# Performance work log

Measured on AMD Instinct MI355X. Metric: run time of the kernel, lower is better.

## Reference

```python
import jax, jax.numpy as jnp
import numpy as np

B, T, IN, H, L, OUT = 64, 512, 128, 256, 3, 50
G = 3 * H  # gate dim (r,z,n)


def setup_inputs() -> dict:
    key = jax.random.key(0)
    ks = jax.random.split(key, 18)
    s = 0.08  # keep gates out of saturation
    r = jax.random.normal
    return {
        "x": r(ks[0], (B, T, IN), jnp.float32),
        "Wih0": r(ks[1], (2, G, IN)) * s,
        "Whh0": r(ks[2], (2, G, H)) * s,
        "bih0": r(ks[3], (2, G)) * s,
        "bhh0": r(ks[4], (2, G)) * s,
        "Wih": r(ks[5], (L - 1, 2, G, 2 * H)) * s,
        "Whh": r(ks[6], (L - 1, 2, G, H)) * s,
        "bih": r(ks[7], (L - 1, 2, G)) * s,
        "bhh": r(ks[8], (L - 1, 2, G)) * s,
        "W1": r(ks[9], (128, 2 * H)) * s,
        "b1": r(ks[10], (128,)) * s,
        "W2": r(ks[11], (64, 128)) * s,
        "b2": r(ks[12], (64,)) * s,
        "W3": r(ks[13], (H, 64)) * s,
        "b3": r(ks[14], (H,)) * s,
        "W4": r(ks[15], (OUT, H)) * s,
        "b4": r(ks[16], (OUT,)) * s,
    }


def _gru_dir(x, Wih, Whh, bih, bhh, reverse):
    # x: [B,T,D]. Precompute input gates with one big GEMM, scan only hidden matmul.
    xg = jnp.einsum('btd,gd->tbg', x, Wih) + bih  # [T,B,3H]
    h0 = jnp.zeros((x.shape[0], H), x.dtype)

    def step(h, xg_t):
        hg = h @ Whh.T + bhh                     # [B,3H]
        xr, xz, xn = jnp.split(xg_t, 3, axis=-1)
        hr, hz, hn = jnp.split(hg, 3, axis=-1)
        r = jax.nn.sigmoid(xr + hr)
        z = jax.nn.sigmoid(xz + hz)
        n = jnp.tanh(xn + r * hn)
        h = (1.0 - z) * n + z * h
        return h, h

    _, ys = jax.lax.scan(step, h0, xg, reverse=reverse)  # ys[t] aligned to time t
    return jnp.transpose(ys, (1, 0, 2))  # [B,T,H]


def reference(x, Wih0, Whh0, bih0, bhh0, Wih, Whh, bih, bhh,
              W1, b1, W2, b2, W3, b3, W4, b4):
    h = x
    for l in range(L):
        if l == 0:
            wi, wh, bi, bh = Wih0, Whh0, bih0, bhh0
        else:
            wi, wh, bi, bh = Wih[l - 1], Whh[l - 1], bih[l - 1], bhh[l - 1]
        fwd = _gru_dir(h, wi[0], wh[0], bi[0], bh[0], False)
        bwd = _gru_dir(h, wi[1], wh[1], bi[1], bh[1], True)
        h = jnp.concatenate([fwd, bwd], axis=-1)  # [B,T,2H]
    last = h[:, -1, :]  # [B,2H]
    y = jax.nn.relu(last @ W1.T + b1)
    y = jax.nn.relu(y @ W2.T + b2)
    y = jax.nn.relu(y @ W3.T + b3)
    return y @ W4.T + b4  # [B,OUT]
```

## Files before the change

### kernel.cpp

```cpp
#include <hip/hip_runtime.h>
#include <stdint.h>

#define B_ 64
#define T_ 512
#define IN_ 128
#define H_ 256
#define G_ 768
#define M0_ (B_*T_)

typedef _Float16 f16;
typedef _Float16 f16x2 __attribute__((ext_vector_type(2)));
typedef _Float16 half8 __attribute__((ext_vector_type(8)));
typedef float f32x4 __attribute__((ext_vector_type(4)));

template<bool AF32>
__global__ __launch_bounds__(256) void k_proj(
    const float* __restrict__ Af, const f16* __restrict__ Ah,
    const float* __restrict__ W, const float* __restrict__ bias,
    f16* __restrict__ out, int K)
{
  int dir = blockIdx.z;
  const float* Wd = W + (size_t)dir*G_*K;
  const float* bd = bias + dir*G_;
  f16* outd = out + (size_t)dir*M0_*G_;
  int m0 = blockIdx.x*128, n0 = blockIdx.y*128;
  int tid = threadIdx.x, lane = tid & 63, wv = tid >> 6;
  int wm = wv >> 1, wn = wv & 1;
  int l15 = lane & 15, quad = lane >> 4;

  __shared__ f16 As[128][72];
  __shared__ f16 Ws[128][72];

  f32x4 acc[4][4];
  #pragma unroll
  for (int i = 0; i < 4; i++)
    #pragma unroll
    for (int j = 0; j < 4; j++) acc[i][j] = (f32x4){0.f,0.f,0.f,0.f};

  int lr = tid >> 3, lk = (tid & 7) * 8;
  for (int k0 = 0; k0 < K; k0 += 64){
    #pragma unroll
    for (int it = 0; it < 4; it++){
      int row = lr + it*32;
      if (AF32){
        const float* p = &Af[(size_t)(m0+row)*K + k0 + lk];
        float4 v0 = *(const float4*)p;
        float4 v1 = *(const float4*)(p + 4);
        *(half8*)&As[row][lk] = (half8){(f16)v0.x,(f16)v0.y,(f16)v0.z,(f16)v0.w,
                                        (f16)v1.x,(f16)v1.y,(f16)v1.z,(f16)v1.w};
      } else {
        *(uint4*)&As[row][lk] = *(const uint4*)&Ah[(size_t)(m0+row)*K + k0 + lk];
      }
      {
        const float* p = &Wd[(size_t)(n0+row)*K + k0 + lk];
        float4 v0 = *(const float4*)p;
        float4 v1 = *(const float4*)(p + 4);
        *(half8*)&Ws[row][lk] = (half8){(f16)v0.x,(f16)v0.y,(f16)v0.z,(f16)v0.w,
                                        (f16)v1.x,(f16)v1.y,(f16)v1.z,(f16)v1.w};
      }
    }
    __syncthreads();
    #pragma unroll
    for (int kk = 0; kk < 64; kk += 32){
      half8 af[4], bf[4];
      #pragma unroll
      for (int mi = 0; mi < 4; mi++) af[mi] = *(const half8*)&As[wm*64 + mi*16 + l15][kk + quad*8];
      #pragma unroll
      for (int ni = 0; ni < 4; ni++) bf[ni] = *(const half8*)&Ws[wn*64 + ni*16 + l15][kk + quad*8];
      #pragma unroll
      for (int mi = 0; mi < 4; mi++)
        #pragma unroll
        for (int ni = 0; ni < 4; ni++)
          acc[mi][ni] = __builtin_amdgcn_mfma_f32_16x16x32_f16(af[mi], bf[ni], acc[mi][ni], 0, 0, 0);
    }
    __syncthreads();
  }
  #pragma unroll
  for (int mi = 0; mi < 4; mi++){
    #pragma unroll
    for (int ni = 0; ni < 4; ni++){
      int m = m0 + wm*64 + mi*16 + quad*4;
      int n = n0 + wn*64 + ni*16 + l15;
      float bn = bd[n];
      #pragma unroll
      for (int r = 0; r < 4; r++)
        outd[(size_t)(m+r)*G_ + n] = (f16)(acc[mi][ni][r] + bn);
    }
  }
}

__global__ __launch_bounds__(256) __attribute__((amdgpu_waves_per_eu(1, 1)))
void k_rnn(
    const f16* __restrict__ xg, const float* __restrict__ whh,
    const float* __restrict__ bhh, f16* __restrict__ y)
{
  int b = blockIdx.x, dir = blockIdx.y;
  int tid = threadIdx.x, lane = tid & 63, wv = tid >> 6;
  int kg = lane >> 4;

  const f16* cxg = xg + ((size_t)dir*M0_ + (size_t)b*T_)*G_;
  const float* wbase = whh + (size_t)dir*G_*H_;
  const float* bh = bhh + dir*G_;
  f16* yb = y + (size_t)b*T_*512 + dir*256;

  __shared__ __align__(16) f16 h0buf[256];
  __shared__ __align__(16) f16 h1buf[256];

  half8 wf[96];
  #pragma unroll
  for (int t = 0; t < 12; t++){
    int g = t >> 2, c = t & 3;
    const float* wrow = wbase + (size_t)(g*256 + wv*64 + c*16 + (lane & 15))*H_;
    #pragma unroll
    for (int kf = 0; kf < 8; kf++){
      const float4* p = (const float4*)(wrow + kf*32 + kg*8);
      float4 v0 = p[0], v1 = p[1];
      wf[t*8+kf] = (half8){(f16)v0.x,(f16)v0.y,(f16)v0.z,(f16)v0.w,
                           (f16)v1.x,(f16)v1.y,(f16)v1.z,(f16)v1.w};
    }
  }

  float br = bh[tid], bz = bh[tid+256], bn = bh[tid+512];
  float hreg = 0.f;
  h0buf[tid] = (f16)0.f;
  __syncthreads();

  f16 axr_, axz_, axn_, bxr_, bxz_, bxn_;

  {
    int t0 = dir ? (T_-1) : 0;
    const f16* xp = cxg + (size_t)t0*G_ + tid;
    axr_ = xp[0]; axz_ = xp[256]; axn_ = xp[512];
  }

#define STEP_BODY(SRC, DST, XR, XZ, XN, TT)                                     \
  {                                                                             \
    const f16* hp = &SRC[kg*8];                                                 \
    f32x4 acc[12];                                                              \
    half8 acur = *(const half8*)hp;                                             \
    half8 anxt = *(const half8*)(hp + 32);                                      \
    _Pragma("unroll")                                                           \
    for (int kf = 0; kf < 8; kf++){                                             \
      half8 ac = acur;                                                          \
      acur = anxt;                                                              \
      if (kf < 6) anxt = *(const half8*)(hp + (kf+2)*32);                       \
      _Pragma("unroll")                                                         \
      for (int t = 0; t < 12; t++){                                             \
        if (kf == 0)                                                            \
          acc[t] = __builtin_amdgcn_mfma_f32_16x16x32_f16(ac, wf[t*8+kf],       \
                     (f32x4){0.f,0.f,0.f,0.f}, 0, 0, 0);                        \
        else                                                                    \
          acc[t] = __builtin_amdgcn_mfma_f32_16x16x32_f16(ac, wf[t*8+kf],       \
                     acc[t], 0, 0, 0);                                          \
      }                                                                         \
    }                                                                           \
    float r0 = (kg & 1) ? acc[1][0] : acc[0][0];                                \
    float r1 = (kg & 1) ? acc[3][0] : acc[2][0];                                \
    float sr = (kg & 2) ? r1 : r0;                                              \
    float z0 = (kg & 1) ? acc[5][0] : acc[4][0];                                \
    float z1 = (kg & 1) ? acc[7][0] : acc[6][0];                                \
    float sz = (kg & 2) ? z1 : z0;                                              \
    float n0v = (kg & 1) ? acc[9][0]  : acc[8][0];                              \
    float n1v = (kg & 1) ? acc[11][0] : acc[10][0];                             \
    float sn = (kg & 2) ? n1v : n0v;                                            \
    float ar = (float)(XR) + sr + br; ar = fminf(fmaxf(ar, -30.f), 30.f);       \
    float az = (float)(XZ) + sz + bz; az = fminf(fmaxf(az, -30.f), 30.f);       \
    float r = 1.f/(1.f + __expf(-ar));                                          \
    float z = 1.f/(1.f + __expf(-az));                                          \
    float an = (float)(XN) + r*(sn + bn); an = fminf(fmaxf(an, -15.f), 15.f);   \
    float e = __expf(2.f*an);                                                   \
    float nn = (e - 1.f)/(e + 1.f);                                             \
    hreg = (1.f - z)*nn + z*hreg;                                               \
    DST[tid] = (f16)hreg;                                                       \
    yb[(size_t)(TT)*512 + tid] = (f16)hreg;                                     \
    asm volatile("s_waitcnt lgkmcnt(0)\n\ts_barrier" ::: "memory");             \
  }

  for (int s = 0; s < T_; s += 2){
    int ttA = dir ? (T_-1-s) : s;
    int ttB = dir ? (T_-2-s) : (s+1);

    {
      const f16* xq = cxg + (size_t)ttB*G_ + tid;
      bxr_ = xq[0]; bxz_ = xq[256]; bxn_ = xq[512];
    }
    STEP_BODY(h0buf, h1buf, axr_, axz_, axn_, ttA)

    {
      int s2 = (s + 2 < T_) ? (s + 2) : (T_ - 1);
      int tt2 = dir ? (T_-1-s2) : s2;
      const f16* xq = cxg + (size_t)tt2*G_ + tid;
      axr_ = xq[0]; axz_ = xq[256]; axn_ = xq[512];
    }
    STEP_BODY(h1buf, h0buf, bxr_, bxz_, bxn_, ttB)
  }
#undef STEP_BODY
}

__global__ __launch_bounds__(256) void k_head(
    const f16* __restrict__ y,
    const float* __restrict__ W1, const float* __restrict__ b1,
    const float* __restrict__ W2, const float* __restrict__ b2,
    const float* __restrict__ W3, const float* __restrict__ b3,
    const float* __restrict__ W4, const float* __restrict__ b4,
    float* __restrict__ out)
{
  int b = blockIdx.x, tid = threadIdx.x;
  __shared__ float a0[512], a1[128], a2[64], a3[256];
  const f16* yr = y + ((size_t)b*T_ + (T_-1))*512;
  a0[tid] = (float)yr[tid]; a0[tid+256] = (float)yr[tid+256];
  __syncthreads();
  if (tid < 128){
    float s = b1[tid];
    const float4* w = (const float4*)(W1 + (size_t)tid*512);
    #pragma unroll 8
    for (int c = 0; c < 128; c++){
      float4 v = w[c];
      s += v.x*a0[c*4] + v.y*a0[c*4+1] + v.z*a0[c*4+2] + v.w*a0[c*4+3];
    }
    a1[tid] = fmaxf(s, 0.f);
  }
  __syncthreads();
  if (tid < 64){
    float s = b2[tid];
    const float4* w = (const float4*)(W2 + (size_t)tid*128);
    #pragma unroll
    for (int c = 0; c < 32; c++){
      float4 v = w[c];
      s += v.x*a1[c*4] + v.y*a1[c*4+1] + v.z*a1[c*4+2] + v.w*a1[c*4+3];
    }
    a2[tid] = fmaxf(s, 0.f);
  }
  __syncthreads();
  if (tid < 256){
    float s = b3[tid];
    const float4* w = (const float4*)(W3 + (size_t)tid*64);
    #pragma unroll
    for (int c = 0; c < 16; c++){
      float4 v = w[c];
      s += v.x*a2[c*4] + v.y*a2[c*4+1] + v.z*a2[c*4+2] + v.w*a2[c*4+3];
    }
    a3[tid] = fmaxf(s, 0.f);
  }
  __syncthreads();
  if (tid < 50){
    float s = b4[tid];
    const float4* w = (const float4*)(W4 + (size_t)tid*256);
    #pragma unroll
    for (int c = 0; c < 64; c++){
      float4 v = w[c];
      s += v.x*a3[c*4] + v.y*a3[c*4+1] + v.z*a3[c*4+2] + v.w*a3[c*4+3];
    }
    out[b*50 + tid] = s;
  }
}

extern "C" void kernel_launch(void* const* d_in, const int* in_sizes, int n_in,
                              void* d_out, int out_size, void* d_ws, size_t ws_size,
                              hipStream_t stream)
{
  const float* x    = (const float*)d_in[0];
  const float* Wih0 = (const float*)d_in[1];
  const float* Whh0 = (const float*)d_in[2];
  const float* bih0 = (const float*)d_in[3];
  const float* bhh0 = (const float*)d_in[4];
  const float* Wih  = (const float*)d_in[5];
  const float* Whh  = (const float*)d_in[6];
  const float* bih  = (const float*)d_in[7];
  const float* bhh  = (const float*)d_in[8];
  const float* W1 = (const float*)d_in[9];
  const float* b1 = (const float*)d_in[10];
  const float* W2 = (const float*)d_in[11];
  const float* b2 = (const float*)d_in[12];
  const float* W3 = (const float*)d_in[13];
  const float* b3 = (const float*)d_in[14];
  const float* W4 = (const float*)d_in[15];
  const float* b4 = (const float*)d_in[16];

  char* ws = (char*)d_ws;
  f16* xg = (f16*)ws;
  f16* y  = (f16*)(ws + 100663296ull);

  k_proj<true ><<<dim3(M0_/128, 6, 2), dim3(256), 0, stream>>>(x, nullptr, Wih0, bih0, xg, IN_);
  k_rnn        <<<dim3(B_, 2),         dim3(256), 0, stream>>>(xg, Whh0, bhh0, y);
  k_proj<false><<<dim3(M0_/128, 6, 2), dim3(256), 0, stream>>>(nullptr, y, Wih, bih, xg, 2*H_);
  k_rnn        <<<dim3(B_, 2),         dim3(256), 0, stream>>>(xg, Whh, bhh, y);
  k_proj<false><<<dim3(M0_/128, 6, 2), dim3(256), 0, stream>>>(nullptr, y, Wih + 1ull*2*G_*(2*H_), bih + 2*G_, xg, 2*H_);
  k_rnn        <<<dim3(B_, 2),         dim3(256), 0, stream>>>(xg, Whh + 1ull*2*G_*H_, bhh + 2*G_, y);

  k_head<<<dim3(B_), dim3(256), 0, stream>>>(y, W1, b1, W2, b2, W3, b3, W4, b4,
                                             (float*)d_out);
}
```

Before: 2.241 ms.

## Replace MFMA recurrent matvec with fdot2 dot products across 512 threads

The recurrent hidden-state matvec in the GRU kernel moves from 16x16x32 MFMA tiles, most of whose output columns were discarded, to per-lane packed fp16 dot2 accumulation. Each block now uses 512 threads (8 waves, two per SIMD). Every lane holds a 64-wide K slice for 6 gate rows, and partial sums are combined with cross-lane shuffles. This removes the wasted matrix-core work in a batch-1 matvec and spreads the weights over more waves, at the cost of shuffle reductions, half the lanes idling during the gate math, and more barrier participants per step.

```diff
diff --git a/kernel.cpp b/kernel.cpp
--- a/kernel.cpp
+++ b/kernel.cpp
@@ -12,6 +12,12 @@
 typedef _Float16 f16x2 __attribute__((ext_vector_type(2)));
 typedef _Float16 half8 __attribute__((ext_vector_type(8)));
 typedef float f32x4 __attribute__((ext_vector_type(4)));
+
+#if __has_builtin(__builtin_amdgcn_fdot2)
+__device__ inline float fdot2f(f16x2 a, f16x2 b, float c){ return __builtin_amdgcn_fdot2(a, b, c, false); }
+#else
+__device__ inline float fdot2f(f16x2 a, f16x2 b, float c){ return c + (float)a.x*(float)b.x + (float)a.y*(float)b.y; }
+#endif
 
 template<bool AF32>
 __global__ __launch_bounds__(256) void k_proj(
@@ -89,14 +95,18 @@
   }
 }
 
-__global__ __launch_bounds__(256) __attribute__((amdgpu_waves_per_eu(1, 1)))
+__global__ __launch_bounds__(512) __attribute__((amdgpu_waves_per_eu(2, 2)))
 void k_rnn(
     const f16* __restrict__ xg, const float* __restrict__ whh,
     const float* __restrict__ bhh, f16* __restrict__ y)
 {
   int b = blockIdx.x, dir = blockIdx.y;
   int tid = threadIdx.x, lane = tid & 63, wv = tid >> 6;
-  int kg = lane >> 4;
+  int g = lane >> 4;
+  int i = lane & 15;
+  int o = lane & 31;
+  int u = wv*32 + o;
+  int dsel = (lane >> 4) & 1;
 
   const f16* cxg = xg + ((size_t)dir*M0_ + (size_t)b*T_)*G_;
   const float* wbase = whh + (size_t)dir*G_*H_;
@@ -106,73 +116,69 @@
   __shared__ __align__(16) f16 h0buf[256];
   __shared__ __align__(16) f16 h1buf[256];
 
-  half8 wf[96];
+  f16x2 wf2[192];
   #pragma unroll
-  for (int t = 0; t < 12; t++){
-    int g = t >> 2, c = t & 3;
-    const float* wrow = wbase + (size_t)(g*256 + wv*64 + c*16 + (lane & 15))*H_;
-    #pragma unroll
-    for (int kf = 0; kf < 8; kf++){
-      const float4* p = (const float4*)(wrow + kf*32 + kg*8);
-      float4 v0 = p[0], v1 = p[1];
-      wf[t*8+kf] = (half8){(f16)v0.x,(f16)v0.y,(f16)v0.z,(f16)v0.w,
-                           (f16)v1.x,(f16)v1.y,(f16)v1.z,(f16)v1.w};
-    }
-  }
-
-  float br = bh[tid], bz = bh[tid+256], bn = bh[tid+512];
+  for (int m = 0; m < 6; m++){
+    int gamma = m >> 1, d = m & 1;
+    const float* wrow = wbase + (size_t)(gamma*256 + wv*32 + i + d*16)*H_ + g*64;
+    #pragma unroll
+    for (int q = 0; q < 16; q++){
+      float4 v = ((const float4*)wrow)[q];
+      wf2[m*32 + q*2 + 0] = (f16x2){(f16)v.x, (f16)v.y};
+      wf2[m*32 + q*2 + 1] = (f16x2){(f16)v.z, (f16)v.w};
+    }
+  }
+
+  float br = bh[u], bz = bh[u+256], bn = bh[u+512];
   float hreg = 0.f;
-  h0buf[tid] = (f16)0.f;
-  __syncthreads();
-
-  f16 axr_, axz_, axn_, bxr_, bxz_, bxn_;
-
+  if (tid < 256) h0buf[tid] = (f16)0.f;
+  __syncthreads();
+
+  f16 axr, axz, axn, bxr, bxz, bxn;
   {
     int t0 = dir ? (T_-1) : 0;
-    const f16* xp = cxg + (size_t)t0*G_ + tid;
-    axr_ = xp[0]; axz_ = xp[256]; axn_ = xp[512];
-  }
-
-#define STEP_BODY(SRC, DST, XR, XZ, XN, TT)                                     \
+    const f16* xp = cxg + (size_t)t0*G_ + u;
+    axr = xp[0]; axz = xp[256]; axn = xp[512];
+  }
+
+#define RSTEP(SRC, DST, XR, XZ, XN, TT)                                         \
   {                                                                             \
-    const f16* hp = &SRC[kg*8];                                                 \
-    f32x4 acc[12];                                                              \
-    half8 acur = *(const half8*)hp;                                             \
-    half8 anxt = *(const half8*)(hp + 32);                                      \
+    const half8* hp = (const half8*)&SRC[g*64];                                 \
+    half8 hv[8];                                                                \
     _Pragma("unroll")                                                           \
-    for (int kf = 0; kf < 8; kf++){                                             \
-      half8 ac = acur;                                                          \
-      acur = anxt;                                                              \
-      if (kf < 6) anxt = *(const half8*)(hp + (kf+2)*32);                       \
+    for (int s2 = 0; s2 < 8; s2++) hv[s2] = hp[s2];                             \
+    float ac[6] = {0.f,0.f,0.f,0.f,0.f,0.f};                                    \
+    _Pragma("unroll")                                                           \
+    for (int s2 = 0; s2 < 8; s2++){                                             \
+      half8 hh = hv[s2];                                                        \
       _Pragma("unroll")                                                         \
-      for (int t = 0; t < 12; t++){                                             \
-        if (kf == 0)                                                            \
-          acc[t] = __builtin_amdgcn_mfma_f32_16x16x32_f16(ac, wf[t*8+kf],       \
-                     (f32x4){0.f,0.f,0.f,0.f}, 0, 0, 0);                        \
-        else                                                                    \
-          acc[t] = __builtin_amdgcn_mfma_f32_16x16x32_f16(ac, wf[t*8+kf],       \
-                     acc[t], 0, 0, 0);                                          \
+      for (int q = 0; q < 4; q++){                                              \
+        f16x2 pp = {hh[2*q], hh[2*q+1]};                                        \
+        _Pragma("unroll")                                                       \
+        for (int m = 0; m < 6; m++)                                             \
+          ac[m] = fdot2f(wf2[m*32 + s2*4 + q], pp, ac[m]);                      \
       }                                                                         \
     }                                                                           \
-    float r0 = (kg & 1) ? acc[1][0] : acc[0][0];                                \
-    float r1 = (kg & 1) ? acc[3][0] : acc[2][0];                                \
-    float sr = (kg & 2) ? r1 : r0;                                              \
-    float z0 = (kg & 1) ? acc[5][0] : acc[4][0];                                \
-    float z1 = (kg & 1) ? acc[7][0] : acc[6][0];                                \
-    float sz = (kg & 2) ? z1 : z0;                                              \
-    float n0v = (kg & 1) ? acc[9][0]  : acc[8][0];                              \
-    float n1v = (kg & 1) ? acc[11][0] : acc[10][0];                             \
-    float sn = (kg & 2) ? n1v : n0v;                                            \
+    _Pragma("unroll")                                                           \
+    for (int m = 0; m < 6; m++){                                                \
+      ac[m] += __shfl_xor(ac[m], 16);                                           \
+      ac[m] += __shfl_xor(ac[m], 32);                                           \
+    }                                                                           \
+    float sr = dsel ? ac[1] : ac[0];                                            \
+    float sz = dsel ? ac[3] : ac[2];                                            \
+    float sn = dsel ? ac[5] : ac[4];                                            \
     float ar = (float)(XR) + sr + br; ar = fminf(fmaxf(ar, -30.f), 30.f);       \
     float az = (float)(XZ) + sz + bz; az = fminf(fmaxf(az, -30.f), 30.f);       \
-    float r = 1.f/(1.f + __expf(-ar));                                          \
-    float z = 1.f/(1.f + __expf(-az));                                          \
-    float an = (float)(XN) + r*(sn + bn); an = fminf(fmaxf(an, -15.f), 15.f);   \
-    float e = __expf(2.f*an);                                                   \
-    float nn = (e - 1.f)/(e + 1.f);                                             \
-    hreg = (1.f - z)*nn + z*hreg;                                               \
-    DST[tid] = (f16)hreg;                                                       \
-    yb[(size_t)(TT)*512 + tid] = (f16)hreg;                                     \
+    float r_ = 1.f/(1.f + __expf(-ar));                                         \
+    float z_ = 1.f/(1.f + __expf(-az));                                         \
+    float an = (float)(XN) + r_*(sn + bn); an = fminf(fmaxf(an, -15.f), 15.f);  \
+    float e_ = __expf(2.f*an);                                                  \
+    float nn = (e_ - 1.f)/(e_ + 1.f);                                           \
+    hreg = (1.f - z_)*nn + z_*hreg;                                             \
+    if (lane < 32){                                                             \
+      DST[u] = (f16)hreg;                                                       \
+      yb[(size_t)(TT)*512 + u] = (f16)hreg;                                     \
+    }                                                                           \
     asm volatile("s_waitcnt lgkmcnt(0)\n\ts_barrier" ::: "memory");             \
   }
 
@@ -181,20 +187,20 @@
     int ttB = dir ? (T_-2-s) : (s+1);
 
     {
-      const f16* xq = cxg + (size_t)ttB*G_ + tid;
-      bxr_ = xq[0]; bxz_ = xq[256]; bxn_ = xq[512];
-    }
-    STEP_BODY(h0buf, h1buf, axr_, axz_, axn_, ttA)
+      const f16* xq = cxg + (size_t)ttB*G_ + u;
+      bxr = xq[0]; bxz = xq[256]; bxn = xq[512];
+    }
+    RSTEP(h0buf, h1buf, axr, axz, axn, ttA)
 
     {
-      int s2 = (s + 2 < T_) ? (s + 2) : (T_ - 1);
-      int tt2 = dir ? (T_-1-s2) : s2;
-      const f16* xq = cxg + (size_t)tt2*G_ + tid;
-      axr_ = xq[0]; axz_ = xq[256]; axn_ = xq[512];
-    }
-    STEP_BODY(h1buf, h0buf, bxr_, bxz_, bxn_, ttB)
-  }
-#undef STEP_BODY
+      int s2c = (s + 2 < T_) ? (s + 2) : (T_ - 1);
+      int tt2 = dir ? (T_-1-s2c) : s2c;
+      const f16* xq = cxg + (size_t)tt2*G_ + u;
+      axr = xq[0]; axz = xq[256]; axn = xq[512];
+    }
+    RSTEP(h1buf, h0buf, bxr, bxz, bxn, ttB)
+  }
+#undef RSTEP
 }
 
 __global__ __launch_bounds__(256) void k_head(
@@ -282,11 +288,11 @@
   f16* y  = (f16*)(ws + 100663296ull);
 
   k_proj<true ><<<dim3(M0_/128, 6, 2), dim3(256), 0, stream>>>(x, nullptr, Wih0, bih0, xg, IN_);
-  k_rnn        <<<dim3(B_, 2),         dim3(256), 0, stream>>>(xg, Whh0, bhh0, y);
+  k_rnn        <<<dim3(B_, 2),         dim3(512), 0, stream>>>(xg, Whh0, bhh0, y);
   k_proj<false><<<dim3(M0_/128, 6, 2), dim3(256), 0, stream>>>(nullptr, y, Wih, bih, xg, 2*H_);
-  k_rnn        <<<dim3(B_, 2),         dim3(256), 0, stream>>>(xg, Whh, bhh, y);
+  k_rnn        <<<dim3(B_, 2),         dim3(512), 0, stream>>>(xg, Whh, bhh, y);
   k_proj<false><<<dim3(M0_/128, 6, 2), dim3(256), 0, stream>>>(nullptr, y, Wih + 1ull*2*G_*(2*H_), bih + 2*G_, xg, 2*H_);
-  k_rnn        <<<dim3(B_, 2),         dim3(256), 0, stream>>>(xg, Whh + 1ull*2*G_*H_, bhh + 2*G_, y);
+  k_rnn        <<<dim3(B_, 2),         dim3(512), 0, stream>>>(xg, Whh + 1ull*2*G_*H_, bhh + 2*G_, y);
 
   k_head<<<dim3(B_), dim3(256), 0, stream>>>(y, W1, b1, W2, b2, W3, b3, W4, b4,
                                              (float*)d_out);
```

New measurement: 2.409 ms. 1.08x slower.

## Batch 16 sequences per RNN block to fill MFMA rows

Applied to the files above, without the earlier changes.

The recurrent GRU kernel now handles 16 batch rows per workgroup instead of one, so every row of the 16x16x32 MFMA A operand holds a real hidden state rather than padding. The grid shrinks from 64x2 to 4x2 blocks, and each thread computes 16 gate outputs per step. Bias is folded into the accumulator initialisation, and the next step's input gates are loaded after the current step. The cost is far less parallelism (8 CUs busy), 16x more elementwise gate math per thread on the serial path, and scattered f16 global loads and stores.

```diff
diff --git a/kernel.cpp b/kernel.cpp
--- a/kernel.cpp
+++ b/kernel.cpp
@@ -94,23 +94,23 @@
     const f16* __restrict__ xg, const float* __restrict__ whh,
     const float* __restrict__ bhh, f16* __restrict__ y)
 {
-  int b = blockIdx.x, dir = blockIdx.y;
+  int bg = blockIdx.x, dir = blockIdx.y;
+  int b0 = bg << 4;
   int tid = threadIdx.x, lane = tid & 63, wv = tid >> 6;
-  int kg = lane >> 4;
-
-  const f16* cxg = xg + ((size_t)dir*M0_ + (size_t)b*T_)*G_;
+  int l15 = lane & 15, kg = lane >> 4;
+
+  const f16* cxg = xg + (size_t)dir*M0_*G_;
   const float* wbase = whh + (size_t)dir*G_*H_;
   const float* bh = bhh + dir*G_;
-  f16* yb = y + (size_t)b*T_*512 + dir*256;
-
-  __shared__ __align__(16) f16 h0buf[256];
-  __shared__ __align__(16) f16 h1buf[256];
+
+  __shared__ __align__(16) f16 h0[16][264];
+  __shared__ __align__(16) f16 h1[16][264];
 
   half8 wf[96];
   #pragma unroll
   for (int t = 0; t < 12; t++){
     int g = t >> 2, c = t & 3;
-    const float* wrow = wbase + (size_t)(g*256 + wv*64 + c*16 + (lane & 15))*H_;
+    const float* wrow = wbase + (size_t)(g*256 + wv*64 + c*16 + l15)*H_;
     #pragma unroll
     for (int kf = 0; kf < 8; kf++){
       const float4* p = (const float4*)(wrow + kf*32 + kg*8);
@@ -120,81 +120,91 @@
     }
   }
 
-  float br = bh[tid], bz = bh[tid+256], bn = bh[tid+512];
-  float hreg = 0.f;
-  h0buf[tid] = (f16)0.f;
-  __syncthreads();
-
-  f16 axr_, axz_, axn_, bxr_, bxz_, bxn_;
-
+  float bias_[12];
+  #pragma unroll
+  for (int t = 0; t < 12; t++){
+    int g = t >> 2, c = t & 3;
+    bias_[t] = bh[g*256 + wv*64 + c*16 + l15];
+  }
+
+  for (int idx = tid; idx < 16*264; idx += 256) ((f16*)h0)[idx] = (f16)0.f;
+  __syncthreads();
+
+  f16 xr_[16], xz_[16], xn_[16];
   {
     int t0 = dir ? (T_-1) : 0;
-    const f16* xp = cxg + (size_t)t0*G_ + tid;
-    axr_ = xp[0]; axz_ = xp[256]; axn_ = xp[512];
-  }
-
-#define STEP_BODY(SRC, DST, XR, XZ, XN, TT)                                     \
+    #pragma unroll
+    for (int r = 0; r < 4; r++){
+      const f16* p = cxg + ((size_t)(b0 + kg*4 + r)*T_ + t0)*G_ + wv*64 + l15;
+      #pragma unroll
+      for (int c = 0; c < 4; c++){
+        xr_[r*4+c] = p[c*16];
+        xz_[r*4+c] = p[256 + c*16];
+        xn_[r*4+c] = p[512 + c*16];
+      }
+    }
+  }
+
+#define RSTEP(SRC, DST, TT, TN)                                                 \
   {                                                                             \
-    const f16* hp = &SRC[kg*8];                                                 \
     f32x4 acc[12];                                                              \
-    half8 acur = *(const half8*)hp;                                             \
-    half8 anxt = *(const half8*)(hp + 32);                                      \
     _Pragma("unroll")                                                           \
     for (int kf = 0; kf < 8; kf++){                                             \
-      half8 ac = acur;                                                          \
-      acur = anxt;                                                              \
-      if (kf < 6) anxt = *(const half8*)(hp + (kf+2)*32);                       \
+      half8 a = *(const half8*)&SRC[l15][kf*32 + kg*8];                         \
       _Pragma("unroll")                                                         \
       for (int t = 0; t < 12; t++){                                             \
         if (kf == 0)                                                            \
-          acc[t] = __builtin_amdgcn_mfma_f32_16x16x32_f16(ac, wf[t*8+kf],       \
-                     (f32x4){0.f,0.f,0.f,0.f}, 0, 0, 0);                        \
+          acc[t] = __builtin_amdgcn_mfma_f32_16x16x32_f16(a, wf[t*8],           \
+                     (f32x4){bias_[t],bias_[t],bias_[t],bias_[t]}, 0, 0, 0);    \
         else                                                                    \
-          acc[t] = __builtin_amdgcn_mfma_f32_16x16x32_f16(ac, wf[t*8+kf],       \
+          acc[t] = __builtin_amdgcn_mfma_f32_16x16x32_f16(a, wf[t*8+kf],        \
                      acc[t], 0, 0, 0);                                          \
       }                                                                         \
     }                                                                           \
-    float r0 = (kg & 1) ? acc[1][0] : acc[0][0];                                \
-    float r1 = (kg & 1) ? acc[3][0] : acc[2][0];                                \
-    float sr = (kg & 2) ? r1 : r0;                                              \
-    float z0 = (kg & 1) ? acc[5][0] : acc[4][0];                                \
-    float z1 = (kg & 1) ? acc[7][0] : acc[6][0];                                \
-    float sz = (kg & 2) ? z1 : z0;                                              \
-    float n0v = (kg & 1) ? acc[9][0]  : acc[8][0];                              \
-    float n1v = (kg & 1) ? acc[11][0] : acc[10][0];                             \
-    float sn = (kg & 2) ? n1v : n0v;                                            \
-    float ar = (float)(XR) + sr + br; ar = fminf(fmaxf(ar, -30.f), 30.f);       \
-    float az = (float)(XZ) + sz + bz; az = fminf(fmaxf(az, -30.f), 30.f);       \
-    float r = 1.f/(1.f + __expf(-ar));                                          \
-    float z = 1.f/(1.f + __expf(-az));                                          \
-    float an = (float)(XN) + r*(sn + bn); an = fminf(fmaxf(an, -15.f), 15.f);   \
-    float e = __expf(2.f*an);                                                   \
-    float nn = (e - 1.f)/(e + 1.f);                                             \
-    hreg = (1.f - z)*nn + z*hreg;                                               \
-    DST[tid] = (f16)hreg;                                                       \
-    yb[(size_t)(TT)*512 + tid] = (f16)hreg;                                     \
+    _Pragma("unroll")                                                           \
+    for (int r = 0; r < 4; r++){                                                \
+      _Pragma("unroll")                                                         \
+      for (int c = 0; c < 4; c++){                                              \
+        float sr = acc[c][r];                         \
+        float sz = acc[4+c][r];                                \
+        float sn = acc[8+c][r];                                \
+        float hprev = (float)SRC[kg*4+r][wv*64 + c*16 + l15];                   \
+        float ar = (float)xr_[r*4+c] + sr; ar = fminf(fmaxf(ar,-30.f),30.f);    \
+        float az = (float)xz_[r*4+c] + sz; az = fminf(fmaxf(az,-30.f),30.f);    \
+        float rg = 1.f/(1.f + __expf(-ar));                                     \
+        float zg = 1.f/(1.f + __expf(-az));                                     \
+        float an = (float)xn_[r*4+c] + rg*sn; an = fminf(fmaxf(an,-15.f),15.f); \
+        float e_ = __expf(2.f*an);                                              \
+        float nn = (e_ - 1.f)/(e_ + 1.f);                                       \
+        float hnew = (1.f - zg)*nn + zg*hprev;                                  \
+        DST[kg*4+r][wv*64 + c*16 + l15] = (f16)hnew;                            \
+        y[((size_t)(b0 + kg*4 + r)*T_ + (TT))*512 + dir*256 + wv*64 + c*16 + l15] \
+            = (f16)hnew;                                                        \
+      }                                                                         \
+    }                                                                           \
+    _Pragma("unroll")                                                           \
+    for (int r = 0; r < 4; r++){      \
+      const f16* p = cxg + ((size_t)(b0 + kg*4 + r)*T_ + (TN))*G_ + wv*64 + l15;\
+      _Pragma("unroll")                                                         \
+      for (int c = 0; c < 4; c++){                                              \
+        xr_[r*4+c] = p[c*16];                                                   \
+        xz_[r*4+c] = p[256 + c*16];                                             \
+        xn_[r*4+c] = p[512 + c*16];                                             \
+      }                                                                         \
+    }                                                                           \
     asm volatile("s_waitcnt lgkmcnt(0)\n\ts_barrier" ::: "memory");             \
   }
 
   for (int s = 0; s < T_; s += 2){
     int ttA = dir ? (T_-1-s) : s;
     int ttB = dir ? (T_-2-s) : (s+1);
-
-    {
-      const f16* xq = cxg + (size_t)ttB*G_ + tid;
-      bxr_ = xq[0]; bxz_ = xq[256]; bxn_ = xq[512];
-    }
-    STEP_BODY(h0buf, h1buf, axr_, axz_, axn_, ttA)
-
-    {
-      int s2 = (s + 2 < T_) ? (s + 2) : (T_ - 1);
-      int tt2 = dir ? (T_-1-s2) : s2;
-      const f16* xq = cxg + (size_t)tt2*G_ + tid;
-      axr_ = xq[0]; axz_ = xq[256]; axn_ = xq[512];
-    }
-    STEP_BODY(h1buf, h0buf, bxr_, bxz_, bxn_, ttB)
-  }
-#undef STEP_BODY
+    int s2c = (s + 2 < T_) ? (s + 2) : (T_ - 1);
+    int ttC = dir ? (T_-1-s2c) : s2c;
+
+    RSTEP(h0, h1, ttA, ttB)
+    RSTEP(h1, h0, ttB, ttC)
+  }
+#undef RSTEP
 }
 
 __global__ __launch_bounds__(256) void k_head(
@@ -282,11 +292,11 @@
   f16* y  = (f16*)(ws + 100663296ull);
 
   k_proj<true ><<<dim3(M0_/128, 6, 2), dim3(256), 0, stream>>>(x, nullptr, Wih0, bih0, xg, IN_);
-  k_rnn        <<<dim3(B_, 2),         dim3(256), 0, stream>>>(xg, Whh0, bhh0, y);
+  k_rnn        <<<dim3(4, 2),          dim3(256), 0, stream>>>(xg, Whh0, bhh0, y);
   k_proj<false><<<dim3(M0_/128, 6, 2), dim3(256), 0, stream>>>(nullptr, y, Wih, bih, xg, 2*H_);
-  k_rnn        <<<dim3(B_, 2),         dim3(256), 0, stream>>>(xg, Whh, bhh, y);
+  k_rnn        <<<dim3(4, 2),          dim3(256), 0, stream>>>(xg, Whh, bhh, y);
   k_proj<false><<<dim3(M0_/128, 6, 2), dim3(256), 0, stream>>>(nullptr, y, Wih + 1ull*2*G_*(2*H_), bih + 2*G_, xg, 2*H_);
-  k_rnn        <<<dim3(B_, 2),         dim3(256), 0, stream>>>(xg, Whh + 1ull*2*G_*H_, bhh + 2*G_, y);
+  k_rnn        <<<dim3(4, 2),          dim3(256), 0, stream>>>(xg, Whh + 1ull*2*G_*H_, bhh + 2*G_, y);
 
   k_head<<<dim3(B_), dim3(256), 0, stream>>>(y, W1, b1, W2, b2, W3, b3, W4, b4,
                                              (float*)d_out);
```

New measurement: 8.418 ms. 3.76x slower.
